# Kernel tuning notes

Measured on AMD Instinct MI355X. Metric: run time of the kernel, lower is better.

The kernel has to match this reference:

```python
import jax, jax.numpy as jnp
import numpy as np

N_NODES = 50000


def _gcn_layer(x, W, b, src, dst, n_nodes):
    # GCNConv: h = D^{-1/2} (A + I) D^{-1/2} (x W) + b, with src/dst already
    # including self-loops.
    h = x @ W  # [N, out]
    deg = jax.ops.segment_sum(jnp.ones(src.shape, x.dtype), dst,
                              num_segments=n_nodes)  # [N]
    dinv = jnp.where(deg > 0, jax.lax.rsqrt(jnp.maximum(deg, 1e-12)), 0.0)
    norm = dinv[src] * dinv[dst]  # [E+N]
    msg = h[src] * norm[:, None]  # gathered + weighted messages
    out = jax.ops.segment_sum(msg, dst, num_segments=n_nodes)  # scatter-add
    return out + b


def setup_inputs() -> dict:
    key = jax.random.key(0)
    k0, k1, k2, k3 = jax.random.split(key, 4)
    d_in, hidden, n_edges = 128, 128, 800000
    x = jax.random.normal(k0, (N_NODES, d_in), dtype=jnp.float32)
    edge_index = jax.random.randint(k1, (2, n_edges), 0, N_NODES, dtype=jnp.int64)
    W1 = jax.random.normal(k2, (d_in, hidden), dtype=jnp.float32) * (1.0 / np.sqrt(d_in))
    b1 = jnp.zeros((hidden,), jnp.float32)
    W2 = jax.random.normal(k3, (hidden, hidden), dtype=jnp.float32) * (1.0 / np.sqrt(hidden))
    b2 = jnp.zeros((hidden,), jnp.float32)
    return {"x": x, "edge_index": edge_index, "W1": W1, "b1": b1,
            "W2": W2, "b2": b2}


def reference(x, edge_index, W1, b1, W2, b2):
    n = x.shape[0]
    loop = jnp.arange(n, dtype=edge_index.dtype)
    src = jnp.concatenate([edge_index[0], loop])  # add self-loops
    dst = jnp.concatenate([edge_index[1], loop])
    h = _gcn_layer(x, W1, b1, src, dst, n)
    h = jax.nn.relu(h)
    # dropout p=0.5 is identity in eval mode (self.training == False)
    h = _gcn_layer(h, W2, b2, src, dst, n)
    return jax.nn.log_softmax(h, axis=1)
```

## Files before the change

### kernel.cpp

```cpp
#include <hip/hip_runtime.h>
#include <math.h>

#define D 128
#define CAP 6144
#define EPB 4096

typedef __attribute__((ext_vector_type(8))) short bf16x8;
typedef __attribute__((ext_vector_type(4))) float f32x4;

__device__ __forceinline__ float bf_lo(unsigned u) { return __uint_as_float(u << 16); }
__device__ __forceinline__ float bf_hi(unsigned u) { return __uint_as_float(u & 0xFFFF0000u); }
__device__ __forceinline__ unsigned pack_bf16(float a, float b) {
    unsigned ua = __float_as_uint(a), ub = __float_as_uint(b);
    ua = (ua + 0x7FFFu + ((ua >> 16) & 1u)) >> 16;
    ub = (ub + 0x7FFFu + ((ub >> 16) & 1u)) >> 16;
    return ua | (ub << 16);
}

__device__ __forceinline__ int edge_at(const void* eidx, int i64, long long pos) {
    return i64 ? (int)((const long long*)eidx)[pos] : ((const int*)eidx)[pos];
}


__global__ void k_init(const int* e32, int* flag, int* bcnt) {
    int t = threadIdx.x;
    bcnt[t] = 0;
    if (t == 0) {
        int f = 1;
        #pragma unroll
        for (int j = 1; j < 32; j += 2)
            if (e32[j] != 0) f = 0;
        *flag = f;
    }
}


__global__ void __launch_bounds__(256) k_prep(const void* eidx, const int* flag,
                                              int* bcnt,
                                              unsigned* __restrict__ binned, int e) {
    __shared__ int hist[256];
    __shared__ int gbase[256];
    __shared__ int lcur[256];
    __shared__ uint2 ed[EPB];
    int b = blockIdx.x, t = threadIdx.x;

    hist[t] = 0;
    lcur[t] = 0;
    __syncthreads();
    long long base = (long long)b * EPB;
    int i64 = *flag;
    #pragma unroll
    for (int k = 0; k < EPB / 256; ++k) {
        long long i = base + k * 256 + t;
        if (i < e) {
            int s = edge_at(eidx, i64, i);
            int d = edge_at(eidx, i64, (long long)e + i);
            ed[k * 256 + t] = make_uint2((unsigned)s, (unsigned)d);
            atomicAdd(&hist[d >> 8], 1);
        }
    }
    __syncthreads();
    int c = hist[t];
    gbase[t] = c ? atomicAdd(&bcnt[t], c) : 0;
    __syncthreads();
    long long rem = e - base;
    int lim = (rem < EPB) ? (int)rem : EPB;
    for (int j = t; j < lim; j += 256) {
        uint2 sd = ed[j];
        int bk = sd.y >> 8;
        int off = gbase[bk] + atomicAdd(&lcur[bk], 1);
        if (off >= CAP) off = CAP - 1;
        binned[(size_t)bk * CAP + off] = sd.x | ((sd.y & 255u) << 17);
    }
}


template <int AF32>
__device__ __forceinline__ void gemm_body(char* lds, int bid, const void* Ain,
                                          const float* __restrict__ Wf,
                                          unsigned* __restrict__ yout, int n) {
    int tid = threadIdx.x;
    #pragma unroll
    for (int it = 0; it < 32; ++it) {
        int idx = tid + it * 256;
        int c = idx & 127, k2 = idx >> 7;
        *(unsigned*)&lds[c * 272 + k2 * 4] =
            pack_bf16(Wf[(k2 * 2) * D + c], Wf[(k2 * 2 + 1) * D + c]);
    }
    int w = tid >> 6, l = tid & 63;
    int row0 = bid * 128;
    int rowA0 = row0 + w * 16 + (l & 15);
    int rowA1 = rowA0 + 64;
    int rA0 = rowA0 < n ? rowA0 : 0;
    int rA1 = rowA1 < n ? rowA1 : 0;
    __syncthreads();

    f32x4 acc[2][8];
    #pragma unroll
    for (int r = 0; r < 2; ++r)
        #pragma unroll
        for (int f = 0; f < 8; ++f) acc[r][f] = (f32x4)0.f;

    #pragma unroll
    for (int s = 0; s < 4; ++s) {
        bf16x8 a0, a1;
        if (AF32) {
            const float* Af = (const float*)Ain;
            const float4* p0 = (const float4*)(Af + (size_t)rA0 * D + ((l >> 4) << 3) + s * 32);
            const float4* p1 = (const float4*)(Af + (size_t)rA1 * D + ((l >> 4) << 3) + s * 32);
            float4 f0 = p0[0], f1 = p0[1], f2 = p1[0], f3 = p1[1];
            uint4 v0, v1;
            v0.x = pack_bf16(f0.x, f0.y); v0.y = pack_bf16(f0.z, f0.w);
            v0.z = pack_bf16(f1.x, f1.y); v0.w = pack_bf16(f1.z, f1.w);
            v1.x = pack_bf16(f2.x, f2.y); v1.y = pack_bf16(f2.z, f2.w);
            v1.z = pack_bf16(f3.x, f3.y); v1.w = pack_bf16(f3.z, f3.w);
            a0 = *(bf16x8*)&v0;
            a1 = *(bf16x8*)&v1;
        } else {
            const char* Ab = (const char*)Ain;
            a0 = *(const bf16x8*)(Ab + (size_t)rA0 * 256 + ((l >> 4) << 4) + s * 64);
            a1 = *(const bf16x8*)(Ab + (size_t)rA1 * 256 + ((l >> 4) << 4) + s * 64);
        }
        int boff = ((l >> 4) << 4) + s * 64;
        #pragma unroll
        for (int f = 0; f < 8; ++f) {
            bf16x8 b = *(const bf16x8*)&lds[(f * 16 + (l & 15)) * 272 + boff];
            acc[0][f] = __builtin_amdgcn_mfma_f32_16x16x32_bf16(a0, b, acc[0][f], 0, 0, 0);
            acc[1][f] = __builtin_amdgcn_mfma_f32_16x16x32_bf16(a1, b, acc[1][f], 0, 0, 0);
        }
    }

    float* fl = (float*)lds;
    #pragma unroll
    for (int r = 0; r < 2; ++r) {
        __syncthreads();
        {
            int rbase = w * 16 + ((l >> 4) << 2);
            #pragma unroll
            for (int f = 0; f < 8; ++f) {
                int c = f * 16 + (l & 15);
                #pragma unroll
                for (int j = 0; j < 4; ++j)
                    fl[(rbase + j) * 132 + c] = acc[r][f][j];
            }
        }
        __syncthreads();
        int row = tid >> 2, cseg = (tid & 3) << 5;
        int gr = row0 + r * 64 + row;
        if (gr < n) {
            uint4* ob = (uint4*)yout + (size_t)gr * 16 + ((tid & 3) << 2);
            #pragma unroll
            for (int q = 0; q < 4; ++q) {
                uint4 v;
                v.x = pack_bf16(fl[row * 132 + cseg + q * 8 + 0], fl[row * 132 + cseg + q * 8 + 1]);
                v.y = pack_bf16(fl[row * 132 + cseg + q * 8 + 2], fl[row * 132 + cseg + q * 8 + 3]);
                v.z = pack_bf16(fl[row * 132 + cseg + q * 8 + 4], fl[row * 132 + cseg + q * 8 + 5]);
                v.w = pack_bf16(fl[row * 132 + cseg + q * 8 + 6], fl[row * 132 + cseg + q * 8 + 7]);
                ob[q] = v;
            }
        }
    }
}


__global__ void __launch_bounds__(256) k_mid(const unsigned* __restrict__ binned,
                                             const int* __restrict__ bcnt,
                                             unsigned* __restrict__ meta,
                                             unsigned* __restrict__ csr64,
                                             const float* __restrict__ x,
                                             const float* __restrict__ W1,
                                             unsigned* __restrict__ y1,
                                             int n, int nb) {
    __shared__ char lds[34816];
    int b = blockIdx.x, t = threadIdx.x;
    if (b >= nb) {
        gemm_body<1>(lds, b - nb, x, W1, y1, n);
        return;
    }
    int* lcur = (int*)lds;
    lcur[t] = 0;
    __syncthreads();

    int cnt = bcnt[b];
    if (cnt > CAP) cnt = CAP;
    unsigned nodebase = (unsigned)b << 8;
    for (int i = t; i < cnt; i += 256) {
        unsigned en = binned[(size_t)b * CAP + i];
        unsigned src = en & 0x1FFFF;
        unsigned dl = en >> 17;
        int pos = atomicAdd(&lcur[dl], 1);
        unsigned node = nodebase + dl;
        if (pos < 64)
            csr64[(size_t)node * 64 + pos] = src;
    }
    __syncthreads();

    int node = b * 256 + t;
    if (node < n) {
        int dv = lcur[t];
        unsigned q = __float2uint_rn(rsqrtf((float)(dv + 1)) * 32767.0f);
        meta[node] = (q << 17) | (unsigned)(dv < 64 ? dv : 64);
    }
}


template <int EPI>
__global__ void __launch_bounds__(256) k_agg(const unsigned* __restrict__ Y,
                                             const unsigned* __restrict__ meta,
                                             const unsigned* __restrict__ csr64,
                                             const float* __restrict__ bias,
                                             void* __restrict__ outp, int n) {
    int node = __builtin_amdgcn_readfirstlane(blockIdx.x * 4 + (threadIdx.x >> 6));
    if (node >= n) return;
    int lane = threadIdx.x & 63;
    unsigned mt = meta[node];
    unsigned us = Y[(size_t)node * 64 + lane];
    const unsigned* cp = csr64 + (size_t)node * 64;

    int cdeg = mt & 0x1FFFF;
    float di = (float)(mt >> 17) * (1.0f / 32767.0f);
    float ax = 0.f, ay = 0.f;

    int k = 0;
    for (; k + 4 <= cdeg; k += 4) {
        unsigned s0 = cp[k + 0], s1 = cp[k + 1], s2 = cp[k + 2], s3 = cp[k + 3];
        unsigned u0 = Y[(size_t)s0 * 64 + lane];
        unsigned u1 = Y[(size_t)s1 * 64 + lane];
        unsigned u2 = Y[(size_t)s2 * 64 + lane];
        unsigned u3 = Y[(size_t)s3 * 64 + lane];
        float q0 = (float)(meta[s0] >> 17);
        float q1 = (float)(meta[s1] >> 17);
        float q2 = (float)(meta[s2] >> 17);
        float q3 = (float)(meta[s3] >> 17);
        ax += q0 * bf_lo(u0) + q1 * bf_lo(u1) + q2 * bf_lo(u2) + q3 * bf_lo(u3);
        ay += q0 * bf_hi(u0) + q1 * bf_hi(u1) + q2 * bf_hi(u2) + q3 * bf_hi(u3);
    }
    for (; k < cdeg; ++k) {
        unsigned s0 = cp[k];
        unsigned u0 = Y[(size_t)s0 * 64 + lane];
        float q0 = (float)(meta[s0] >> 17);
        ax += q0 * bf_lo(u0);
        ay += q0 * bf_hi(u0);
    }

    float sc = di * (1.0f / 32767.0f);
    float dd = di * di;
    float2 bv = ((const float2*)bias)[lane];
    float z0 = ax * sc + dd * bf_lo(us) + bv.x;
    float z1 = ay * sc + dd * bf_hi(us) + bv.y;

    if (EPI == 0) {
        ((unsigned*)outp)[(size_t)node * 64 + lane] =
            pack_bf16(fmaxf(z0, 0.f), fmaxf(z1, 0.f));
    } else {
        float m = fmaxf(z0, z1);
        #pragma unroll
        for (int off = 1; off < 64; off <<= 1) m = fmaxf(m, __shfl_xor(m, off));
        float s = __expf(z0 - m) + __expf(z1 - m);
        #pragma unroll
        for (int off = 1; off < 64; off <<= 1) s += __shfl_xor(s, off);
        float lse = m + __logf(s);
        ((float2*)outp)[(size_t)node * 64 + lane] = make_float2(z0 - lse, z1 - lse);
    }
}


__global__ void __launch_bounds__(256) k_gemm2(const unsigned* __restrict__ h,
                                               const float* __restrict__ W2,
                                               unsigned* __restrict__ y2, int n) {
    __shared__ char lds[34816];
    gemm_body<0>(lds, blockIdx.x, h, W2, y2, n);
}


extern "C" void kernel_launch(void* const* d_in, const int* in_sizes, int n_in,
                              void* d_out, int out_size, void* d_ws, size_t ws_size,
                              hipStream_t stream) {
    const float* x  = (const float*)d_in[0];
    const void* eix = d_in[1];
    const float* W1 = (const float*)d_in[2];
    const float* b1 = (const float*)d_in[3];
    const float* W2 = (const float*)d_in[4];
    const float* b2 = (const float*)d_in[5];
    float* out = (float*)d_out;
    int n = in_sizes[0] / D;
    int e = in_sizes[1] / 2;

    char* p = (char*)d_ws;
    auto carve = [&](size_t bytes) -> void* {
        void* r = (void*)p;
        p += (bytes + 255) & ~(size_t)255;
        return r;
    };
    int*      flag   = (int*)carve(4);
    unsigned* meta   = (unsigned*)carve((size_t)n * 4);
    int*      bcnt   = (int*)carve(1024);
    unsigned* csr64  = (unsigned*)carve((size_t)n * 64 * 4);
    unsigned* binned = (unsigned*)carve((size_t)256 * CAP * 4);
    unsigned* y1     = (unsigned*)carve((size_t)n * 64 * 4);
    unsigned* h      = (unsigned*)carve((size_t)n * 64 * 4);

    int nb = (n + 255) / 256;
    int ebk = (e + EPB - 1) / EPB;
    int gb = (n + 127) / 128;
    int ab = (n + 3) / 4;

    k_init<<<1, 256, 0, stream>>>((const int*)eix, flag, bcnt);
    k_prep<<<ebk, 256, 0, stream>>>(eix, flag, bcnt, binned, e);
    k_mid<<<nb + gb, 256, 0, stream>>>(binned, bcnt, meta, csr64, x, W1, y1, n, nb);
    k_agg<0><<<ab, 256, 0, stream>>>(y1, meta, csr64, b1, h, n);
    k_gemm2<<<gb, 256, 0, stream>>>(h, W2, y1, n);
    k_agg<1><<<ab, 256, 0, stream>>>(y1, meta, csr64, b2, out, n);
}
```

Measured before the change: 137.8 us.

## Prescale GEMM output by source norm and pad CSR rows to groups of 16

The source-side normalization dinv[src] is folded into the GEMM epilogue, so aggregation no longer gathers meta[src] for each edge. The CSR rows are padded to multiples of 16 using a zero sentinel row, and the aggregation loop runs in fixed 16-wide groups with all indices loaded before the gathers. To make meta available to GEMM1, the fused binning+GEMM1 kernel is split into two launches, which costs an extra launch and removes the overlap between binning and GEMM1. Padding also adds wasted gathers of the zero row.

```diff
diff --git a/kernel.cpp b/kernel.cpp
--- a/kernel.cpp
+++ b/kernel.cpp
@@ -22,9 +22,12 @@
 }
 
 
-__global__ void k_init(const int* e32, int* flag, int* bcnt) {
+__global__ void k_init(const int* e32, int* flag, int* bcnt,
+                       unsigned* y1, unsigned* h, int n) {
     int t = threadIdx.x;
     bcnt[t] = 0;
+    if (t < 64) y1[(size_t)n * 64 + t] = 0;
+    else if (t < 128) h[(size_t)n * 64 + (t - 64)] = 0;
     if (t == 0) {
         int f = 1;
         #pragma unroll
@@ -75,9 +78,47 @@
 }
 
 
+__global__ void __launch_bounds__(256) k_binB(const unsigned* __restrict__ binned,
+                                              const int* __restrict__ bcnt,
+                                              unsigned* __restrict__ meta,
+                                              unsigned* __restrict__ csr64,
+                                              int n) {
+    __shared__ int lcur[256];
+    int b = blockIdx.x, t = threadIdx.x;
+    lcur[t] = 0;
+    __syncthreads();
+
+    int cnt = bcnt[b];
+    if (cnt > CAP) cnt = CAP;
+    unsigned nodebase = (unsigned)b << 8;
+    for (int i = t; i < cnt; i += 256) {
+        unsigned en = binned[(size_t)b * CAP + i];
+        unsigned src = en & 0x1FFFF;
+        unsigned dl = en >> 17;
+        int pos = atomicAdd(&lcur[dl], 1);
+        unsigned node = nodebase + dl;
+        if (pos < 64)
+            csr64[(size_t)node * 64 + pos] = src;
+    }
+    __syncthreads();
+
+    int node = b * 256 + t;
+    if (node < n) {
+        int dv = lcur[t];
+        int filled = dv < 64 ? dv : 64;
+        int pend = (filled + 15) & ~15;
+        for (int j = filled; j < pend; ++j)
+            csr64[(size_t)node * 64 + j] = (unsigned)n;
+        unsigned q = __float2uint_rn(rsqrtf((float)(dv + 1)) * 32767.0f);
+        meta[node] = (q << 17) | (unsigned)(pend >> 4);
+    }
+}
+
+
 template <int AF32>
 __device__ __forceinline__ void gemm_body(char* lds, int bid, const void* Ain,
                                           const float* __restrict__ Wf,
+                                          const unsigned* __restrict__ meta,
                                           unsigned* __restrict__ yout, int n) {
     int tid = threadIdx.x;
     #pragma unroll
@@ -148,59 +189,35 @@
         int row = tid >> 2, cseg = (tid & 3) << 5;
         int gr = row0 + r * 64 + row;
         if (gr < n) {
+            float di = (float)(meta[gr] >> 17) * (1.0f / 32767.0f);
             uint4* ob = (uint4*)yout + (size_t)gr * 16 + ((tid & 3) << 2);
             #pragma unroll
             for (int q = 0; q < 4; ++q) {
                 uint4 v;
-                v.x = pack_bf16(fl[row * 132 + cseg + q * 8 + 0], fl[row * 132 + cseg + q * 8 + 1]);
-                v.y = pack_bf16(fl[row * 132 + cseg + q * 8 + 2], fl[row * 132 + cseg + q * 8 + 3]);
-                v.z = pack_bf16(fl[row * 132 + cseg + q * 8 + 4], fl[row * 132 + cseg + q * 8 + 5]);
-                v.w = pack_bf16(fl[row * 132 + cseg + q * 8 + 6], fl[row * 132 + cseg + q * 8 + 7]);
+                v.x = pack_bf16(di * fl[row * 132 + cseg + q * 8 + 0], di * fl[row * 132 + cseg + q * 8 + 1]);
+                v.y = pack_bf16(di * fl[row * 132 + cseg + q * 8 + 2], di * fl[row * 132 + cseg + q * 8 + 3]);
+                v.z = pack_bf16(di * fl[row * 132 + cseg + q * 8 + 4], di * fl[row * 132 + cseg + q * 8 + 5]);
+                v.w = pack_bf16(di * fl[row * 132 + cseg + q * 8 + 6], di * fl[row * 132 + cseg + q * 8 + 7]);
                 ob[q] = v;
             }
         }
     }
 }
 
-
-__global__ void __launch_bounds__(256) k_mid(const unsigned* __restrict__ binned,
-                                             const int* __restrict__ bcnt,
-                                             unsigned* __restrict__ meta,
-                                             unsigned* __restrict__ csr64,
-                                             const float* __restrict__ x,
-                                             const float* __restrict__ W1,
-                                             unsigned* __restrict__ y1,
-                                             int n, int nb) {
+__global__ void __launch_bounds__(256) k_gemm1(const float* __restrict__ x,
+                                               const float* __restrict__ W1,
+                                               const unsigned* __restrict__ meta,
+                                               unsigned* __restrict__ y1, int n) {
     __shared__ char lds[34816];
-    int b = blockIdx.x, t = threadIdx.x;
-    if (b >= nb) {
-        gemm_body<1>(lds, b - nb, x, W1, y1, n);
-        return;
-    }
-    int* lcur = (int*)lds;
-    lcur[t] = 0;
-    __syncthreads();
-
-    int cnt = bcnt[b];
-    if (cnt > CAP) cnt = CAP;
-    unsigned nodebase = (unsigned)b << 8;
-    for (int i = t; i < cnt; i += 256) {
-        unsigned en = binned[(size_t)b * CAP + i];
-        unsigned src = en & 0x1FFFF;
-        unsigned dl = en >> 17;
-        int pos = atomicAdd(&lcur[dl], 1);
-        unsigned node = nodebase + dl;
-        if (pos < 64)
-            csr64[(size_t)node * 64 + pos] = src;
-    }
-    __syncthreads();
-
-    int node = b * 256 + t;
-    if (node < n) {
-        int dv = lcur[t];
-        unsigned q = __float2uint_rn(rsqrtf((float)(dv + 1)) * 32767.0f);
-        meta[node] = (q << 17) | (unsigned)(dv < 64 ? dv : 64);
-    }
+    gemm_body<1>(lds, blockIdx.x, x, W1, meta, y1, n);
+}
+
+__global__ void __launch_bounds__(256) k_gemm2(const unsigned* __restrict__ h,
+                                               const float* __restrict__ W2,
+                                               const unsigned* __restrict__ meta,
+                                               unsigned* __restrict__ y2, int n) {
+    __shared__ char lds[34816];
+    gemm_body<0>(lds, blockIdx.x, h, W2, meta, y2, n);
 }
 
 
@@ -217,37 +234,31 @@
     unsigned us = Y[(size_t)node * 64 + lane];
     const unsigned* cp = csr64 + (size_t)node * 64;
 
-    int cdeg = mt & 0x1FFFF;
+    int gcnt = mt & 7;
     float di = (float)(mt >> 17) * (1.0f / 32767.0f);
     float ax = 0.f, ay = 0.f;
 
-    int k = 0;
-    for (; k + 4 <= cdeg; k += 4) {
-        unsigned s0 = cp[k + 0], s1 = cp[k + 1], s2 = cp[k + 2], s3 = cp[k + 3];
-        unsigned u0 = Y[(size_t)s0 * 64 + lane];
-        unsigned u1 = Y[(size_t)s1 * 64 + lane];
-        unsigned u2 = Y[(size_t)s2 * 64 + lane];
-        unsigned u3 = Y[(size_t)s3 * 64 + lane];
-        float q0 = (float)(meta[s0] >> 17);
-        float q1 = (float)(meta[s1] >> 17);
-        float q2 = (float)(meta[s2] >> 17);
-        float q3 = (float)(meta[s3] >> 17);
-        ax += q0 * bf_lo(u0) + q1 * bf_lo(u1) + q2 * bf_lo(u2) + q3 * bf_lo(u3);
-        ay += q0 * bf_hi(u0) + q1 * bf_hi(u1) + q2 * bf_hi(u2) + q3 * bf_hi(u3);
-    }
-    for (; k < cdeg; ++k) {
-        unsigned s0 = cp[k];
-        unsigned u0 = Y[(size_t)s0 * 64 + lane];
-        float q0 = (float)(meta[s0] >> 17);
-        ax += q0 * bf_lo(u0);
-        ay += q0 * bf_hi(u0);
-    }
-
-    float sc = di * (1.0f / 32767.0f);
-    float dd = di * di;
+#define GRP(base)                                                       \
+    {                                                                   \
+        unsigned sv[16];                                                \
+        _Pragma("unroll") for (int k2 = 0; k2 < 16; ++k2)               \
+            sv[k2] = cp[(base) + k2];                                   \
+        _Pragma("unroll") for (int k2 = 0; k2 < 16; ++k2) {             \
+            unsigned u = Y[(size_t)sv[k2] * 64 + lane];                 \
+            ax += bf_lo(u);                                             \
+            ay += bf_hi(u);                                             \
+        }                                                               \
+    }
+
+    if (gcnt > 0) GRP(0);
+    if (gcnt > 1) GRP(16);
+    if (gcnt > 2) GRP(32);
+    if (gcnt > 3) GRP(48);
+#undef GRP
+
     float2 bv = ((const float2*)bias)[lane];
-    float z0 = ax * sc + dd * bf_lo(us) + bv.x;
-    float z1 = ay * sc + dd * bf_hi(us) + bv.y;
+    float z0 = di * (ax + bf_lo(us)) + bv.x;
+    float z1 = di * (ay + bf_hi(us)) + bv.y;
 
     if (EPI == 0) {
         ((unsigned*)outp)[(size_t)node * 64 + lane] =
@@ -262,14 +273,6 @@
         float lse = m + __logf(s);
         ((float2*)outp)[(size_t)node * 64 + lane] = make_float2(z0 - lse, z1 - lse);
     }
-}
-
-
-__global__ void __launch_bounds__(256) k_gemm2(const unsigned* __restrict__ h,
-                                               const float* __restrict__ W2,
-                                               unsigned* __restrict__ y2, int n) {
-    __shared__ char lds[34816];
-    gemm_body<0>(lds, blockIdx.x, h, W2, y2, n);
 }
 
 
@@ -293,22 +296,23 @@
         return r;
     };
     int*      flag   = (int*)carve(4);
-    unsigned* meta   = (unsigned*)carve((size_t)n * 4);
+    unsigned* meta   = (unsigned*)carve((size_t)(n + 1) * 4);
     int*      bcnt   = (int*)carve(1024);
     unsigned* csr64  = (unsigned*)carve((size_t)n * 64 * 4);
     unsigned* binned = (unsigned*)carve((size_t)256 * CAP * 4);
-    unsigned* y1     = (unsigned*)carve((size_t)n * 64 * 4);
-    unsigned* h      = (unsigned*)carve((size_t)n * 64 * 4);
+    unsigned* y1     = (unsigned*)carve((size_t)(n + 1) * 64 * 4);
+    unsigned* h      = (unsigned*)carve((size_t)(n + 1) * 64 * 4);
 
     int nb = (n + 255) / 256;
     int ebk = (e + EPB - 1) / EPB;
     int gb = (n + 127) / 128;
     int ab = (n + 3) / 4;
 
-    k_init<<<1, 256, 0, stream>>>((const int*)eix, flag, bcnt);
+    k_init<<<1, 256, 0, stream>>>((const int*)eix, flag, bcnt, y1, h, n);
     k_prep<<<ebk, 256, 0, stream>>>(eix, flag, bcnt, binned, e);
-    k_mid<<<nb + gb, 256, 0, stream>>>(binned, bcnt, meta, csr64, x, W1, y1, n, nb);
+    k_binB<<<nb, 256, 0, stream>>>(binned, bcnt, meta, csr64, n);
+    k_gemm1<<<gb, 256, 0, stream>>>(x, W1, meta, y1, n);
     k_agg<0><<<ab, 256, 0, stream>>>(y1, meta, csr64, b1, h, n);
-    k_gemm2<<<gb, 256, 0, stream>>>(h, W2, y1, n);
+    k_gemm2<<<gb, 256, 0, stream>>>(h, W2, meta, y1, n);
     k_agg<1><<<ab, 256, 0, stream>>>(y1, meta, csr64, b2, out, n);
 }
```

Result: faster. 135.1 us (-2.0%).
